# Kernel tuning notes

Hardware: AMD Instinct MI355X
Metric: run time of the kernel (lower is better)

Reference implementation:

```python
import jax, jax.numpy as jnp
import numpy as np

N_ATOMS = 20000
N_EDGES = 320000
NC = 16
N_RBF = 8
LOMAX = 2
CUTOFF = 4.0

# TensorProductLayer(max_x_way=2, max_y_way=2, max_z_way=2) combination list
TP_COMBOS = [(xw, yw, zw) for xw in range(3) for yw in range(3)
             for zw in range(abs(yw - xw), min(2, xw + yw) + 1, 2)]


def _aggregate(x, y, xw, yw, zw):
    # Contract the last c Cartesian dims of x with the first c Cartesian dims of y.
    # x: [E, nc] + (3,)*xw ; y: [E, nc] + (3,)*yw -> [E, nc] + (3,)*zw
    c = (xw + yw - zw) // 2
    E, nc = x.shape[0], x.shape[1]
    xa = x.reshape(E, nc, 3 ** (xw - c), 3 ** c)
    yb = y.reshape(E, nc, 3 ** c, 3 ** (yw - c))
    out = jnp.einsum('enak,enkb->enab', xa, yb)
    return out.reshape((E, nc) + (3,) * zw)


def _channel_linear(t, W, b=None):
    # nn.Linear applied over the channel dim (dim 1) of [B, nc] + (3,)*l tensors
    out = jnp.einsum('ec...,oc->eo...', t, W)
    if b is not None:
        out = out + b.reshape((1, -1) + (1,) * (t.ndim - 2))
    return out


def _forward(edge_index, positions, feats0, feats1, feats2, bessel_w, rbf_w,
             rbf_b, lin1_w, lin1_b, lin2_w, lin2_b, act_w, act_b, n_atoms):
    idx_i = edge_index[0]
    idx_j = edge_index[1]
    # find_distances
    rij = positions[idx_j] - positions[idx_i]              # [E,3]
    dij = jnp.sqrt(jnp.sum(rij * rij, axis=-1))            # [E]
    uij = rij / dij[:, None]                               # unit vectors
    # RBF: trainable BesselRBF * PolynomialCutoff(p=6)
    d = dij[:, None]                                       # [E,1]
    radial = jnp.sqrt(2.0 / CUTOFF) * jnp.sin(bessel_w * d) / d   # [E,n_rbf]
    t = d / CUTOFF
    poly = 1.0 - 28.0 * t**6 + 48.0 * t**7 - 21.0 * t**8
    env = jnp.where(t < 1.0, poly, 0.0)
    rbf_ij = radial * env                                  # [E,n_rbf]
    E = dij.shape[0]
    # find_moment(l): outer powers of the unit vector
    moments = [jnp.ones((E,), dij.dtype), uij, uij[:, :, None] * uij[:, None, :]]
    feats = [feats0, feats1, feats2]
    # gather neighbor feats + tensor linear mixing (bias only for l=0)
    x = {}
    for l in range(LOMAX + 1):
        g = feats[l][idx_j]
        x[l] = _channel_linear(g, lin1_w[l], lin1_b if l == 0 else None)
    # radial filters times moments
    y = {}
    for l in range(LOMAX + 1):
        fn = rbf_ij @ rbf_w[l].T + rbf_b[l]                # [E,nc]
        fn = fn.reshape((E, NC) + (1,) * l)                # expand_to(fn, l+2)
        y[l] = jnp.expand_dims(moments[l], 1) * fn         # [E,nc]+(3,)*l
    # equivariant tensor product
    msgs = {}
    for xw, yw, zw in TP_COMBOS:
        m = _aggregate(x[xw], y[yw], xw, yw, zw)
        msgs[zw] = msgs[zw] + m if zw in msgs else m
    # scatter-add aggregation per receiving node
    node_msg = {l: jax.ops.segment_sum(msgs[l], idx_i, num_segments=n_atoms)
                for l in range(LOMAX + 1)}
    # message processing: TensorLinearMixing -> TensorActivation
    out = {}
    for l in range(LOMAX + 1):
        h = _channel_linear(node_msg[l], lin2_w[l], lin2_b if l == 0 else None)
        if l == 0:
            out[l] = jax.nn.silu(h)
        else:
            flat = h.reshape(h.shape[0], h.shape[1], -1)
            norm = act_w[l - 1] * jnp.sum(flat * flat, axis=2) + act_b[l - 1]
            factor = jax.nn.sigmoid(norm).reshape(norm.shape + (1,) * l)
            out[l] = factor * h
    # residual update of node feats
    return (feats0 + out[0], feats1 + out[1], feats2 + out[2])


def setup_inputs() -> dict:
    key = jax.random.key(0)
    ks = jax.random.split(key, 16)
    positions = jax.random.uniform(ks[0], (N_ATOMS, 3), jnp.float32) * 5.0
    idx_i = jax.random.randint(ks[1], (N_EDGES,), 0, N_ATOMS)
    off = jax.random.randint(ks[2], (N_EDGES,), 1, N_ATOMS)
    idx_j = (idx_i + off) % N_ATOMS                        # guarantees i != j
    edge_index = jnp.stack([idx_i, idx_j]).astype(jnp.int32)
    atomic_numbers = jax.random.randint(ks[3], (N_ATOMS,), 1, 100)
    feats0 = jax.random.normal(ks[4], (N_ATOMS, NC), jnp.float32)
    feats1 = jax.random.normal(ks[5], (N_ATOMS, NC, 3), jnp.float32) * 0.3
    feats2 = jax.random.normal(ks[6], (N_ATOMS, NC, 3, 3), jnp.float32) * 0.3
    bessel_w = jnp.arange(1, N_RBF + 1, dtype=jnp.float32) * jnp.pi / CUTOFF
    s_rbf = 1.0 / np.sqrt(N_RBF)
    s_nc = 1.0 / np.sqrt(NC)
    rbf_w = jax.random.normal(ks[7], (3, NC, N_RBF), jnp.float32) * s_rbf
    rbf_b = jax.random.normal(ks[8], (3, NC), jnp.float32) * s_rbf
    lin1_w = jax.random.normal(ks[9], (3, NC, NC), jnp.float32) * s_nc
    lin1_b = jax.random.normal(ks[10], (NC,), jnp.float32) * s_nc
    lin2_w = jax.random.normal(ks[11], (3, NC, NC), jnp.float32) * s_nc
    lin2_b = jax.random.normal(ks[12], (NC,), jnp.float32) * s_nc
    act_w = jnp.ones((2, NC), jnp.float32)
    act_b = jnp.zeros((2, NC), jnp.float32)
    return {
        'edge_index': edge_index, 'positions': positions,
        'atomic_numbers': atomic_numbers,
        'feats0': feats0, 'feats1': feats1, 'feats2': feats2,
        'bessel_w': bessel_w, 'rbf_w': rbf_w, 'rbf_b': rbf_b,
        'lin1_w': lin1_w, 'lin1_b': lin1_b, 'lin2_w': lin2_w,
        'lin2_b': lin2_b, 'act_w': act_w, 'act_b': act_b,
    }


def reference(edge_index, positions, atomic_numbers, feats0, feats1, feats2,
              bessel_w, rbf_w, rbf_b, lin1_w, lin1_b, lin2_w, lin2_b,
              act_w, act_b):
    n_atoms = atomic_numbers.shape[0]
    return _forward(edge_index, positions, feats0, feats1, feats2, bessel_w,
                    rbf_w, rbf_b, lin1_w, lin1_b, lin2_w, lin2_b, act_w,
                    act_b, n_atoms)
```

## Files before the change

kernel.cpp:

```cpp
#include <hip/hip_runtime.h>
#include <math.h>

#define N_ATOMS 20000
#define N_EDGES 320000
#define NC 16
#define N_RBF 8
#define CUTOFF 4.0f
#define CAP 48

__device__ __forceinline__ unsigned bf16pair(float a, float b) {
    unsigned ua = __float_as_uint(a);
    ua = (ua + 0x7FFFu + ((ua >> 16) & 1u)) >> 16;
    unsigned ub = __float_as_uint(b);
    ub = (ub + 0x7FFFu + ((ub >> 16) & 1u)) >> 16;
    return ua | (ub << 16);
}
__device__ __forceinline__ float bflo(unsigned w) { return __uint_as_float(w << 16); }
__device__ __forceinline__ float bfhi(unsigned w) { return __uint_as_float(w & 0xFFFF0000u); }


__global__ __launch_bounds__(256) void pre_kernel(
    const int* __restrict__ idx_i, const int* __restrict__ idx_j,
    const float* __restrict__ pos, const float* __restrict__ f0,
    const float* __restrict__ f1, const float* __restrict__ f2,
    const float* __restrict__ w1, const float* __restrict__ b1,
    int* __restrict__ cnt, float4* __restrict__ jgeom, uint4* __restrict__ xgb) {
    int tid = threadIdx.x;
    int b = blockIdx.x;
    if (b < 1250) {
        int al = tid >> 4;
        int o = tid & 15;
        int a = b * 16 + al;

        float w10[NC], w11[NC], w12[NC];
#pragma unroll
        for (int c = 0; c < NC; c++) {
            w10[c] = w1[0 * 256 + o * 16 + c];
            w11[c] = w1[1 * 256 + o * 16 + c];
            w12[c] = w1[2 * 256 + o * 16 + c];
        }
        const float4* G0 = (const float4*)(f0 + a * 16);
        const float4* G1 = (const float4*)(f1 + a * 48);
        const float4* G2 = (const float4*)(f2 + a * 144);
        float x0 = b1[o];
#pragma unroll
        for (int v = 0; v < 4; v++) {
            float4 q = G0[v];
            const float* qf = (const float*)&q;
#pragma unroll
            for (int t = 0; t < 4; t++) x0 += w10[4 * v + t] * qf[t];
        }
        float v1[3] = {0.f, 0.f, 0.f};
#pragma unroll
        for (int v = 0; v < 12; v++) {
            float4 q = G1[v];
            const float* qf = (const float*)&q;
#pragma unroll
            for (int t = 0; t < 4; t++) {
                int p = 4 * v + t;
                v1[p % 3] += w11[p / 3] * qf[t];
            }
        }
        float M[9] = {0.f, 0.f, 0.f, 0.f, 0.f, 0.f, 0.f, 0.f, 0.f};
#pragma unroll
        for (int v = 0; v < 36; v++) {
            float4 q = G2[v];
            const float* qf = (const float*)&q;
#pragma unroll
            for (int t = 0; t < 4; t++) {
                int p = 4 * v + t;
                M[p % 9] += w12[p / 9] * qf[t];
            }
        }
        uint4 lo, hi;
        lo.x = bf16pair(x0, v1[0]);
        lo.y = bf16pair(v1[1], v1[2]);
        lo.z = bf16pair(M[0], M[1]);
        lo.w = bf16pair(M[2], M[3]);
        hi.x = bf16pair(M[4], M[5]);
        hi.y = bf16pair(M[6], M[7]);
        hi.z = bf16pair(M[8], 0.f);
        hi.w = 0u;
        size_t base = ((size_t)a * 16 + o) * 2;
        xgb[base] = lo;
        xgb[base + 1] = hi;
    } else {
        int e = (b - 1250) * 256 + tid;
        int i = idx_i[e];
        int j = idx_j[e];
        int p = atomicAdd(&cnt[i], 1);
        if (p < CAP) {
            float dx = pos[j * 3 + 0] - pos[i * 3 + 0];
            float dy = pos[j * 3 + 1] - pos[i * 3 + 1];
            float dz = pos[j * 3 + 2] - pos[i * 3 + 2];
            float4 g;
            g.x = dx; g.y = dy; g.z = dz; g.w = __int_as_float(j);
            jgeom[i * CAP + p] = g;
        }
    }
}


__global__ __launch_bounds__(256) void main_kernel(
    const int* __restrict__ cnt, const float4* __restrict__ jgeom,
    const uint4* __restrict__ xgb, const float* __restrict__ f0,
    const float* __restrict__ f1, const float* __restrict__ f2,
    const float* __restrict__ bessel_w, const float* __restrict__ rbf_w,
    const float* __restrict__ rbf_b, const float* __restrict__ w2,
    const float* __restrict__ b2, const float* __restrict__ act_w,
    const float* __restrict__ act_b, float* __restrict__ out) {
    int tid = threadIdx.x;
    int lane = tid & 63;
    int wv = tid >> 6;
    int s = lane >> 4;
    int o = lane & 15;
    int a = blockIdx.x * 4 + wv;

    float rw0[N_RBF], rw1[N_RBF], rw2[N_RBF];
#pragma unroll
    for (int k = 0; k < N_RBF; k++) {
        rw0[k] = rbf_w[0 * 128 + o * 8 + k];
        rw1[k] = rbf_w[1 * 128 + o * 8 + k];
        rw2[k] = rbf_w[2 * 128 + o * 8 + k];
    }
    float rb0 = rbf_b[o], rb1 = rbf_b[16 + o], rb2 = rbf_b[32 + o];
    float bw0 = bessel_w[0];
    int deg = cnt[a];
    if (deg > CAP) deg = CAP;
    int base = a * CAP;

    float nm0 = 0.f;
    float nm1[3] = {0.f, 0.f, 0.f};
    float nm2[9] = {0.f, 0.f, 0.f, 0.f, 0.f, 0.f, 0.f, 0.f, 0.f};

    int p = s;
    bool act = p < deg;
    int pn = p + 4;
    bool actn = pn < deg;
    float4 G = make_float4(0, 0, 0, 0), Gn = G;
    uint4 XA = make_uint4(0, 0, 0, 0), XB = XA;
    if (act) {
        G = jgeom[base + p];
        size_t xb = ((size_t)__float_as_int(G.w) * 16 + o) * 2;
        XA = xgb[xb];
        XB = xgb[xb + 1];
    }
    if (actn) Gn = jgeom[base + pn];

    while (__any(act)) {
        int pnn = pn + 4;
        bool actnn = pnn < deg;
        float4 Gnn = make_float4(0, 0, 0, 0);
        if (actnn) Gnn = jgeom[base + pnn];
        uint4 XAn = make_uint4(0, 0, 0, 0), XBn = XAn;
        if (actn) {
            size_t xb = ((size_t)__float_as_int(Gn.w) * 16 + o) * 2;
            XAn = xgb[xb];
            XBn = xgb[xb + 1];
        }
        if (act) {
            float dx = G.x, dy = G.y, dz = G.z;
            float d2 = dx * dx + dy * dy + dz * dz;
            float rs = __builtin_amdgcn_rsqf(d2);
            float d = d2 * rs;
            float ux = dx * rs, uy = dy * rs, uz = dz * rs;

            float t = d * (1.0f / CUTOFF);
            float t3 = t * t * t, t6 = t3 * t3;
            float poly = 1.0f + t6 * (-28.0f + t * (48.0f - 21.0f * t));
            float env = (t < 1.0f) ? poly : 0.0f;
            float pref = 0.70710678118654752f * rs * env;

            float sx, cx;
            __sincosf(bw0 * d, &sx, &cx);
            float tw = 2.0f * cx;
            float sp = 0.f, sc = sx;
            float fn0 = rb0, fn1 = rb1, fn2 = rb2;
#pragma unroll
            for (int k = 0; k < N_RBF; k++) {
                float rv = pref * sc;
                fn0 += rw0[k] * rv;
                fn1 += rw1[k] * rv;
                fn2 += rw2[k] * rv;
                float nx = tw * sc - sp;
                sp = sc;
                sc = nx;
            }

            float x0 = bflo(XA.x);
            float v1x = bfhi(XA.x), v1y = bflo(XA.y), v1z = bfhi(XA.y);
            float M[9] = {bflo(XA.z), bfhi(XA.z), bflo(XA.w), bfhi(XA.w),
                          bflo(XB.x), bfhi(XB.x), bflo(XB.y), bfhi(XB.y),
                          bflo(XB.z)};

            float d1 = v1x * ux + v1y * uy + v1z * uz;
            float Wv[3];
            Wv[0] = M[0] * ux + M[1] * uy + M[2] * uz;
            Wv[1] = M[3] * ux + M[4] * uy + M[5] * uz;
            Wv[2] = M[6] * ux + M[7] * uy + M[8] * uz;
            float q2 = Wv[0] * ux + Wv[1] * uy + Wv[2] * uz;

            nm0 += fn0 * x0 + fn1 * d1 + fn2 * q2;
            float u[3] = {ux, uy, uz};
            float vv[3] = {v1x, v1y, v1z};
#pragma unroll
            for (int b = 0; b < 3; b++)
                nm1[b] += fn0 * vv[b] + fn1 * (x0 * u[b] + Wv[b]) + fn2 * d1 * u[b];
#pragma unroll
            for (int ai = 0; ai < 3; ai++) {
                float coef = fn1 * vv[ai] + fn2 * (x0 * u[ai] + Wv[ai]);
#pragma unroll
                for (int b = 0; b < 3; b++)
                    nm2[ai * 3 + b] += fn0 * M[ai * 3 + b] + coef * u[b];
            }
        }
        p = pn; act = actn; G = Gn; XA = XAn; XB = XBn;
        pn = pnn; actn = actnn; Gn = Gnn;
    }

#pragma unroll
    for (int mask = 16; mask <= 32; mask <<= 1) {
        nm0 += __shfl_xor(nm0, mask, 64);
#pragma unroll
        for (int k = 0; k < 3; k++) nm1[k] += __shfl_xor(nm1[k], mask, 64);
#pragma unroll
        for (int k = 0; k < 9; k++) nm2[k] += __shfl_xor(nm2[k], mask, 64);
    }

    float W0[16], WR[16];
    {
        const float4* wr0 = (const float4*)(w2 + 0 * 256 + o * 16);
        const float* wsel = (s == 0) ? (w2 + 1 * 256 + o * 16) : (w2 + 2 * 256 + o * 16);
        const float4* wrs = (const float4*)wsel;
#pragma unroll
        for (int v = 0; v < 4; v++) {
            *(float4*)&W0[4 * v] = wr0[v];
            *(float4*)&WR[4 * v] = wrs[v];
        }
    }
    float src0, src1, src2;
    if (s == 0) { src0 = nm1[0]; src1 = nm1[1]; src2 = nm1[2]; }
    else if (s == 1) { src0 = nm2[0]; src1 = nm2[1]; src2 = nm2[2]; }
    else if (s == 2) { src0 = nm2[3]; src1 = nm2[4]; src2 = nm2[5]; }
    else { src0 = nm2[6]; src1 = nm2[7]; src2 = nm2[8]; }

    float h0 = b2[o];
    float h[3] = {0.f, 0.f, 0.f};
#pragma unroll
    for (int c = 0; c < 16; c++) {
        h0 += W0[c] * __shfl(nm0, c, 16);
        float t0 = __shfl(src0, c, 16);
        float t1 = __shfl(src1, c, 16);
        float t2 = __shfl(src2, c, 16);
        h[0] += WR[c] * t0;
        h[1] += WR[c] * t1;
        h[2] += WR[c] * t2;
    }

    float sq = h[0] * h[0] + h[1] * h[1] + h[2] * h[2];
    float ss1 = (s == 0) ? sq : 0.f;
    float ss2 = (s == 0) ? 0.f : sq;
    ss1 += __shfl_xor(ss1, 16, 64);
    ss1 += __shfl_xor(ss1, 32, 64);
    ss2 += __shfl_xor(ss2, 16, 64);
    ss2 += __shfl_xor(ss2, 32, 64);
    float n1 = act_w[o] * ss1 + act_b[o];
    float g1f = 1.0f / (1.0f + expf(-n1));
    float n2 = act_w[16 + o] * ss2 + act_b[16 + o];
    float g2f = 1.0f / (1.0f + expf(-n2));

    if (s == 0) {
        float sig0 = 1.0f / (1.0f + expf(-h0));
        out[a * 16 + o] = f0[a * 16 + o] + h0 * sig0;
        int base1 = N_ATOMS * NC + a * 48 + o * 3;
#pragma unroll
        for (int k = 0; k < 3; k++)
            out[base1 + k] = f1[a * 48 + o * 3 + k] + g1f * h[k];
    } else {
        int k0 = (s - 1) * 3;
        int base2 = N_ATOMS * NC * 4 + a * 144 + o * 9 + k0;
#pragma unroll
        for (int t = 0; t < 3; t++)
            out[base2 + t] = f2[a * 144 + o * 9 + k0 + t] + g2f * h[t];
    }
}

extern "C" void kernel_launch(void* const* d_in, const int* in_sizes, int n_in,
                              void* d_out, int out_size, void* d_ws, size_t ws_size,
                              hipStream_t stream) {
    const int* edge_index = (const int*)d_in[0];
    const int* idx_i = edge_index;
    const int* idx_j = edge_index + N_EDGES;
    const float* pos = (const float*)d_in[1];
    const float* f0 = (const float*)d_in[3];
    const float* f1 = (const float*)d_in[4];
    const float* f2 = (const float*)d_in[5];
    const float* bessel_w = (const float*)d_in[6];
    const float* rbf_w = (const float*)d_in[7];
    const float* rbf_b = (const float*)d_in[8];
    const float* w1 = (const float*)d_in[9];
    const float* b1 = (const float*)d_in[10];
    const float* w2 = (const float*)d_in[11];
    const float* b2 = (const float*)d_in[12];
    const float* aw = (const float*)d_in[13];
    const float* ab = (const float*)d_in[14];
    float* out = (float*)d_out;

    int* cnt = (int*)d_ws;
    float4* jgeom = (float4*)(cnt + 20480);
    uint4* xgb = (uint4*)(jgeom + (size_t)N_ATOMS * CAP);

    hipMemsetAsync(cnt, 0, N_ATOMS * sizeof(int), stream);
    pre_kernel<<<2500, 256, 0, stream>>>(idx_i, idx_j, pos, f0, f1, f2, w1, b1,
                                         cnt, jgeom, xgb);
    main_kernel<<<N_ATOMS / 4, 256, 0, stream>>>(cnt, jgeom, xgb, f0, f1, f2,
                                                 bessel_w, rbf_w, rbf_b, w2, b2,
                                                 aw, ab, out);
}
```

Before: 92.23 us.

## Store neighbor indices only and compute edge vectors from padded positions in main kernel

The edge bucketing pass now writes only the neighbor index per slot instead of a float4 holding the displacement and index, and the atom pass writes a padded float4 copy of positions. The main kernel loads each neighbor's position and subtracts the center atom's position itself. The prefetch pipeline is deepened to three stages: index, then position and features, then compute. This cuts the bucketing pass's scattered writes and the workspace traffic, at the cost of an extra dependent gather per edge in the main loop.

```diff
diff --git a/kernel.cpp b/kernel.cpp
--- a/kernel.cpp
+++ b/kernel.cpp
@@ -24,7 +24,8 @@
     const float* __restrict__ pos, const float* __restrict__ f0,
     const float* __restrict__ f1, const float* __restrict__ f2,
     const float* __restrict__ w1, const float* __restrict__ b1,
-    int* __restrict__ cnt, float4* __restrict__ jgeom, uint4* __restrict__ xgb) {
+    int* __restrict__ cnt, int* __restrict__ jslot,
+    float4* __restrict__ pos4, uint4* __restrict__ xgb) {
     int tid = threadIdx.x;
     int b = blockIdx.x;
     if (b < 1250) {
@@ -84,31 +85,27 @@
         size_t base = ((size_t)a * 16 + o) * 2;
         xgb[base] = lo;
         xgb[base + 1] = hi;
+        if (o == 0)
+            pos4[a] = make_float4(pos[a * 3 + 0], pos[a * 3 + 1], pos[a * 3 + 2], 0.f);
     } else {
         int e = (b - 1250) * 256 + tid;
         int i = idx_i[e];
         int j = idx_j[e];
         int p = atomicAdd(&cnt[i], 1);
-        if (p < CAP) {
-            float dx = pos[j * 3 + 0] - pos[i * 3 + 0];
-            float dy = pos[j * 3 + 1] - pos[i * 3 + 1];
-            float dz = pos[j * 3 + 2] - pos[i * 3 + 2];
-            float4 g;
-            g.x = dx; g.y = dy; g.z = dz; g.w = __int_as_float(j);
-            jgeom[i * CAP + p] = g;
-        }
+        if (p < CAP) jslot[i * CAP + p] = j;
     }
 }
 
 
 __global__ __launch_bounds__(256) void main_kernel(
-    const int* __restrict__ cnt, const float4* __restrict__ jgeom,
-    const uint4* __restrict__ xgb, const float* __restrict__ f0,
-    const float* __restrict__ f1, const float* __restrict__ f2,
-    const float* __restrict__ bessel_w, const float* __restrict__ rbf_w,
-    const float* __restrict__ rbf_b, const float* __restrict__ w2,
-    const float* __restrict__ b2, const float* __restrict__ act_w,
-    const float* __restrict__ act_b, float* __restrict__ out) {
+    const int* __restrict__ cnt, const int* __restrict__ jslot,
+    const float4* __restrict__ pos4, const uint4* __restrict__ xgb,
+    const float* __restrict__ f0, const float* __restrict__ f1,
+    const float* __restrict__ f2, const float* __restrict__ bessel_w,
+    const float* __restrict__ rbf_w, const float* __restrict__ rbf_b,
+    const float* __restrict__ w2, const float* __restrict__ b2,
+    const float* __restrict__ act_w, const float* __restrict__ act_b,
+    float* __restrict__ out) {
     int tid = threadIdx.x;
     int lane = tid & 63;
     int wv = tid >> 6;
@@ -125,6 +122,7 @@
     }
     float rb0 = rbf_b[o], rb1 = rbf_b[16 + o], rb2 = rbf_b[32 + o];
     float bw0 = bessel_w[0];
+    float4 pa = pos4[a];
     int deg = cnt[a];
     if (deg > CAP) deg = CAP;
     int base = a * CAP;
@@ -133,33 +131,40 @@
     float nm1[3] = {0.f, 0.f, 0.f};
     float nm2[9] = {0.f, 0.f, 0.f, 0.f, 0.f, 0.f, 0.f, 0.f, 0.f};
 
-    int p = s;
-    bool act = p < deg;
-    int pn = p + 4;
-    bool actn = pn < deg;
-    float4 G = make_float4(0, 0, 0, 0), Gn = G;
-    uint4 XA = make_uint4(0, 0, 0, 0), XB = XA;
-    if (act) {
-        G = jgeom[base + p];
-        size_t xb = ((size_t)__float_as_int(G.w) * 16 + o) * 2;
-        XA = xgb[xb];
-        XB = xgb[xb + 1];
-    }
-    if (actn) Gn = jgeom[base + pn];
-
-    while (__any(act)) {
-        int pnn = pn + 4;
-        bool actnn = pnn < deg;
-        float4 Gnn = make_float4(0, 0, 0, 0);
-        if (actnn) Gnn = jgeom[base + pnn];
-        uint4 XAn = make_uint4(0, 0, 0, 0), XBn = XAn;
-        if (actn) {
-            size_t xb = ((size_t)__float_as_int(Gn.w) * 16 + o) * 2;
-            XAn = xgb[xb];
-            XBn = xgb[xb + 1];
-        }
-        if (act) {
-            float dx = G.x, dy = G.y, dz = G.z;
+    int p1 = s + 4, p2 = s + 8;
+    bool a0 = s < deg, a1 = p1 < deg, a2 = p2 < deg;
+    int j0 = a0 ? jslot[base + s] : 0;
+    int j1 = a1 ? jslot[base + p1] : 0;
+    int j2 = a2 ? jslot[base + p2] : 0;
+    float4 P0 = make_float4(0, 0, 0, 0), P1 = P0;
+    uint4 XA0 = make_uint4(0, 0, 0, 0), XB0 = XA0, XA1 = XA0, XB1 = XA0;
+    if (a0) {
+        P0 = pos4[j0];
+        size_t xb = ((size_t)j0 * 16 + o) * 2;
+        XA0 = xgb[xb];
+        XB0 = xgb[xb + 1];
+    }
+    if (a1) {
+        P1 = pos4[j1];
+        size_t xb = ((size_t)j1 * 16 + o) * 2;
+        XA1 = xgb[xb];
+        XB1 = xgb[xb + 1];
+    }
+
+    while (__any(a0)) {
+        int p3 = p2 + 4;
+        bool a3 = p3 < deg;
+        int j3 = a3 ? jslot[base + p3] : 0;
+        float4 P2 = make_float4(0, 0, 0, 0);
+        uint4 XA2 = make_uint4(0, 0, 0, 0), XB2 = XA2;
+        if (a2) {
+            P2 = pos4[j2];
+            size_t xb = ((size_t)j2 * 16 + o) * 2;
+            XA2 = xgb[xb];
+            XB2 = xgb[xb + 1];
+        }
+        if (a0) {
+            float dx = P0.x - pa.x, dy = P0.y - pa.y, dz = P0.z - pa.z;
             float d2 = dx * dx + dy * dy + dz * dz;
             float rs = __builtin_amdgcn_rsqf(d2);
             float d = d2 * rs;
@@ -187,11 +192,11 @@
                 sc = nx;
             }
 
-            float x0 = bflo(XA.x);
-            float v1x = bfhi(XA.x), v1y = bflo(XA.y), v1z = bfhi(XA.y);
-            float M[9] = {bflo(XA.z), bfhi(XA.z), bflo(XA.w), bfhi(XA.w),
-                          bflo(XB.x), bfhi(XB.x), bflo(XB.y), bfhi(XB.y),
-                          bflo(XB.z)};
+            float x0 = bflo(XA0.x);
+            float v1x = bfhi(XA0.x), v1y = bflo(XA0.y), v1z = bfhi(XA0.y);
+            float M[9] = {bflo(XA0.z), bfhi(XA0.z), bflo(XA0.w), bfhi(XA0.w),
+                          bflo(XB0.x), bfhi(XB0.x), bflo(XB0.y), bfhi(XB0.y),
+                          bflo(XB0.z)};
 
             float d1 = v1x * ux + v1y * uy + v1z * uz;
             float Wv[3];
@@ -204,18 +209,22 @@
             float u[3] = {ux, uy, uz};
             float vv[3] = {v1x, v1y, v1z};
 #pragma unroll
-            for (int b = 0; b < 3; b++)
-                nm1[b] += fn0 * vv[b] + fn1 * (x0 * u[b] + Wv[b]) + fn2 * d1 * u[b];
+            for (int bb = 0; bb < 3; bb++)
+                nm1[bb] += fn0 * vv[bb] + fn1 * (x0 * u[bb] + Wv[bb]) + fn2 * d1 * u[bb];
 #pragma unroll
             for (int ai = 0; ai < 3; ai++) {
                 float coef = fn1 * vv[ai] + fn2 * (x0 * u[ai] + Wv[ai]);
 #pragma unroll
-                for (int b = 0; b < 3; b++)
-                    nm2[ai * 3 + b] += fn0 * M[ai * 3 + b] + coef * u[b];
+                for (int bb = 0; bb < 3; bb++)
+                    nm2[ai * 3 + bb] += fn0 * M[ai * 3 + bb] + coef * u[bb];
             }
         }
-        p = pn; act = actn; G = Gn; XA = XAn; XB = XBn;
-        pn = pnn; actn = actnn; Gn = Gnn;
+        a0 = a1; a1 = a2; a2 = a3;
+        j0 = j1; j1 = j2; j2 = j3;
+        p2 = p3;
+        P0 = P1; P1 = P2;
+        XA0 = XA1; XA1 = XA2;
+        XB0 = XB1; XB1 = XB2;
     }
 
 #pragma unroll
@@ -307,13 +316,14 @@
     float* out = (float*)d_out;
 
     int* cnt = (int*)d_ws;
-    float4* jgeom = (float4*)(cnt + 20480);
-    uint4* xgb = (uint4*)(jgeom + (size_t)N_ATOMS * CAP);
+    int* jslot = cnt + 20480;
+    float4* pos4 = (float4*)(jslot + (size_t)N_ATOMS * CAP);
+    uint4* xgb = (uint4*)(pos4 + N_ATOMS);
 
     hipMemsetAsync(cnt, 0, N_ATOMS * sizeof(int), stream);
     pre_kernel<<<2500, 256, 0, stream>>>(idx_i, idx_j, pos, f0, f1, f2, w1, b1,
-                                         cnt, jgeom, xgb);
-    main_kernel<<<N_ATOMS / 4, 256, 0, stream>>>(cnt, jgeom, xgb, f0, f1, f2,
+                                         cnt, jslot, pos4, xgb);
+    main_kernel<<<N_ATOMS / 4, 256, 0, stream>>>(cnt, jslot, pos4, xgb, f0, f1, f2,
                                                  bessel_w, rbf_w, rbf_b, w2, b2,
                                                  aw, ab, out);
 }
```

After: 97.11 us. +5.3%, slower.
